# Performance work log

Hardware: AMD Instinct MI355X
Metric: run time of the kernel (lower is better)

The kernel has to match this reference:

```python
import jax, jax.numpy as jnp
import numpy as np

B, C, OUTC, H, W, K, P, S = 4, 64, 64, 128, 128, 3, 1, 1
KK = K * K


def setup_inputs() -> dict:
    key = jax.random.key(0)
    ks = jax.random.split(key, 5)
    x = jax.random.normal(ks[0], (B, C, H, W), dtype=jnp.float32)
    # small-scale offset weights keep learned offsets in a realistic few-pixel range
    w_off = jax.random.normal(ks[1], (2 * KK, C, 3, 3), dtype=jnp.float32) * 0.05
    b_off = jnp.zeros((2 * KK,), dtype=jnp.float32)
    w_mask = jax.random.normal(ks[2], (KK, C, 3, 3), dtype=jnp.float32) * 0.05
    b_mask = jnp.zeros((KK,), dtype=jnp.float32)
    w_dcn = jax.random.normal(ks[3], (OUTC, C, K, K), dtype=jnp.float32) * (1.0 / np.sqrt(C * KK))
    b_dcn = jnp.zeros((OUTC,), dtype=jnp.float32)
    return {"x": x, "w_off": w_off, "b_off": b_off, "w_mask": w_mask,
            "b_mask": b_mask, "w_dcn": w_dcn, "b_dcn": b_dcn}


def _conv3x3(x, w, b):
    y = jax.lax.conv_general_dilated(x, w, (1, 1), ((1, 1), (1, 1)),
                                     dimension_numbers=("NCHW", "OIHW", "NCHW"))
    return y + b[None, :, None, None]


def _deform_conv(x, offset, mask, w, b):
    # torchvision DeformConv2d (v2, modulated). offset layout: [B, kk, (dy,dx), H, W]
    Ho = (H + 2 * P - K) // S + 1
    Wo = (W + 2 * P - K) // S + 1
    off = offset.reshape(B, KK, 2, Ho, Wo)
    dy, dx = off[:, :, 0], off[:, :, 1]                      # [B,kk,Ho,Wo]
    ki, kj = jnp.meshgrid(jnp.arange(K), jnp.arange(K), indexing="ij")
    ki = ki.reshape(KK).astype(jnp.float32)
    kj = kj.reshape(KK).astype(jnp.float32)
    hg = (jnp.arange(Ho) * S - P).astype(jnp.float32)
    wg = (jnp.arange(Wo) * S - P).astype(jnp.float32)
    py = dy + ki[None, :, None, None] + hg[None, None, :, None]   # sample y coord
    px = dx + kj[None, :, None, None] + wg[None, None, None, :]   # sample x coord

    y0f = jnp.floor(py)
    x0f = jnp.floor(px)
    ly = py - y0f
    lx = px - x0f
    y0 = y0f.astype(jnp.int32)
    x0 = x0f.astype(jnp.int32)

    x_flat = x.reshape(B, C, H * W)

    def sample(yi, xi, wgt):
        valid = (yi >= 0) & (yi < H) & (xi >= 0) & (xi < W)
        idx = jnp.clip(yi, 0, H - 1) * W + jnp.clip(xi, 0, W - 1)  # [B,kk,Ho,Wo]
        g = jax.vmap(lambda xb, ib: xb[:, ib])(x_flat, idx)        # [B,C,kk,Ho,Wo]
        return g * (wgt * valid)[:, None]

    acc = (sample(y0, x0, (1 - ly) * (1 - lx))
           + sample(y0, x0 + 1, (1 - ly) * lx)
           + sample(y0 + 1, x0, ly * (1 - lx))
           + sample(y0 + 1, x0 + 1, ly * lx))                      # [B,C,kk,Ho,Wo]
    acc = acc * mask.reshape(B, 1, KK, Ho, Wo)
    out = jnp.einsum("bckhw,ock->bohw", acc, w.reshape(OUTC, C, KK))
    return out + b[None, :, None, None]


def reference(x, w_off, b_off, w_mask, b_mask, w_dcn, b_dcn):
    offset = _conv3x3(x, w_off, b_off)
    mask = jax.nn.sigmoid(_conv3x3(x, w_mask, b_mask))
    out = _deform_conv(x, offset, mask, w_dcn, b_dcn)
    return out, offset
```

## Files before the change

### kernel.cpp

```cpp
#include <hip/hip_runtime.h>
#include <hip/hip_bf16.h>
#include <math.h>

#define BB 4
#define CC 64
#define OCN 64
#define HH 128
#define WW 128
#define HW (HH*WW)
#define KKN 9
#define APAD 200

typedef short short8 __attribute__((ext_vector_type(8)));
typedef short short4v __attribute__((ext_vector_type(4)));
typedef float floatx4 __attribute__((ext_vector_type(4)));
typedef unsigned int uintx4 __attribute__((ext_vector_type(4)));

__device__ __forceinline__ float bf2f_us(unsigned short u) {
    return __uint_as_float(((unsigned)u) << 16);
}
__device__ __forceinline__ short f2bfs(float f) {
    __hip_bfloat16 h = __float2bfloat16(f);
    return *reinterpret_cast<short*>(&h);
}
__device__ __forceinline__ uintx4 as_u4(short8 v) {
    union { short8 s; uintx4 u; } x; x.s = v; return x.u;
}
__device__ __forceinline__ float blo(unsigned d) { return __uint_as_float(d << 16); }
__device__ __forceinline__ float bhi(unsigned d) { return __uint_as_float(d & 0xffff0000u); }

__global__ __launch_bounds__(256) void transpose_prep(
    const float* __restrict__ x,
    const float* __restrict__ w_dcn, const float* __restrict__ w_off,
    const float* __restrict__ b_off, const float* __restrict__ w_mask,
    const float* __restrict__ b_mask,
    __hip_bfloat16* __restrict__ xt, __hip_bfloat16* __restrict__ wTf,
    __hip_bfloat16* __restrict__ wOf, float* __restrict__ rebias)
{
    int blk = blockIdx.x;
    int tid = threadIdx.x;
    if (blk < BB * 512) {
        __shared__ float tile[64][33];
        int pixbase = (blk & 511) * 32;
        int b       = blk >> 9;
        const float* xb = x + (size_t)b * CC * HW;
        int p = tid & 31;
        #pragma unroll
        for (int i = 0; i < 8; ++i) {
            int c = (tid >> 5) * 8 + i;
            tile[c][p] = xb[(size_t)c * HW + pixbase + p];
        }
        __syncthreads();
        __hip_bfloat16* xo = xt + ((size_t)b * HW + pixbase) * CC;
        int pixl = tid >> 3;
        int c8t  = tid & 7;
        short8 o;
        #pragma unroll
        for (int i = 0; i < 8; ++i) o[i] = f2bfs(tile[c8t * 8 + i][pixl]);
        *reinterpret_cast<short8*>(&xo[(size_t)pixl * CC + c8t * 8]) = o;
        return;
    }
    int i = (blk - BB * 512) * 256 + tid;
    if (i < 18 * 4 * 64 * 8) {
        int jj = i & 7;
        int l  = (i >> 3) & 63;
        int nt = (i >> 9) & 3;
        int s  = i >> 11;
        int oc = nt * 16 + (l & 15);
        int kk = s * 32 + ((l >> 4) << 3) + jj;
        int c  = kk & 63;
        int kt = kk >> 6;
        wTf[i] = __float2bfloat16(w_dcn[(oc * CC + c) * 9 + kt]);
    }
    int j = i - 18 * 4 * 64 * 8;
    if (j >= 0 && j < 18 * 2 * 64 * 8) {
        int jj = j & 7;
        int l  = (j >> 3) & 63;
        int nt = (j >> 9) & 1;
        int s  = j >> 10;
        int oc = nt * 16 + (l & 15);
        int kk = s * 32 + ((l >> 4) << 3) + jj;
        int c  = kk & 63;
        int kt = kk >> 6;
        float v = 0.0f;
        if (oc < 18)      v = w_off[(oc * CC + c) * 9 + kt];
        else if (oc < 27) v = w_mask[((oc - 18) * CC + c) * 9 + kt];
        wOf[j] = __float2bfloat16(v);
    }
    int r = j - 18 * 2 * 64 * 8;
    if (r >= 0 && r < 27) rebias[r] = (r < 18) ? b_off[r] : b_mask[r - 18];
}

__global__ __launch_bounds__(256, 4) void deform_fused(
    const __hip_bfloat16* __restrict__ xt,
    const __hip_bfloat16* __restrict__ wTf, const __hip_bfloat16* __restrict__ wOf,
    const float* __restrict__ rebias, const float* __restrict__ b_dcn,
    float* __restrict__ off_out, float* __restrict__ out)
{
    __shared__ __align__(16) __hip_bfloat16 accs[64][APAD];
    __shared__ uintx4 tabs[KKN][64];
    __shared__ __hip_bfloat16 offs_l[18][68];
    __shared__ __hip_bfloat16 ms_l[KKN][68];

    int tid    = threadIdx.x;
    int lane   = tid & 63;
    int wv     = __builtin_amdgcn_readfirstlane(tid >> 6);
    int lane15 = lane & 15;
    int lq     = lane >> 4;
    int nt     = wv & 1;
    int ph     = wv >> 1;
    int pix    = tid >> 3;
    int c8     = tid & 7;
    int co     = c8 * 16;
    int kreg   = lq << 3;

    int wo0 = (blockIdx.x & 1) * 64;
    int row = (blockIdx.x >> 1) & (HH - 1);
    int b   = blockIdx.x >> 8;

    const char* xtb = (const char*)(xt + (size_t)b * HW * CC);
    const short8* wTf8 = (const short8*)wTf;
    const short8* wOf8 = (const short8*)wOf;
    const short8 zero8 = {0,0,0,0,0,0,0,0};

    floatx4 accomA[2] = {{0,0,0,0},{0,0,0,0}};
    for (int chunk = 0; chunk < 3; ++chunk) {
        int y = row + chunk - 1;
        bool yvalid = (unsigned)y < (unsigned)HH;
        int yc = min(max(y, 0), HH - 1);
        short8 v[2][3];
        #pragma unroll
        for (int h = 0; h < 2; ++h) {
            #pragma unroll
            for (int kl = 0; kl < 3; ++kl) {
                int xw = wo0 + h * 32 + pix + kl - 1;
                bool valid = yvalid && ((unsigned)xw < (unsigned)WW);
                int xc = min(max(xw, 0), WW - 1);
                short8 t = *(const short8*)(xtb + (((yc * WW) + xc) << 7) + co);
                v[h][kl] = valid ? t : zero8;
            }
        }
        #pragma unroll
        for (int h = 0; h < 2; ++h)
            #pragma unroll
            for (int kl = 0; kl < 3; ++kl)
                *reinterpret_cast<short8*>(&accs[h * 32 + pix][kl * 64 + c8 * 8]) = v[h][kl];
        __syncthreads();

        #pragma unroll
        for (int step = 0; step < 6; ++step) {
            int s = chunk * 6 + step;
            short8 bfrag = wOf8[(size_t)(s * 2 + nt) * 64 + lane];
            #pragma unroll
            for (int q = 0; q < 2; ++q) {
                int pg = ph * 2 + q;
                short8 a = *reinterpret_cast<const short8*>(&accs[pg * 16 + lane15][step * 32 + kreg]);
                accomA[q] = __builtin_amdgcn_mfma_f32_16x16x32_bf16(a, bfrag, accomA[q], 0, 0, 0);
            }
        }
        __syncthreads();
    }

    #pragma unroll
    for (int q = 0; q < 2; ++q) {
        int pg = ph * 2 + q;
        int pcl = pg * 16 + lq * 4;
        int oc = nt * 16 + lane15;
        if (oc < 18) {
            float bias = rebias[oc];
            floatx4 o = accomA[q];
            o[0] += bias; o[1] += bias; o[2] += bias; o[3] += bias;
            *reinterpret_cast<floatx4*>(
                &off_out[(((size_t)b * 18 + oc) * HH + row) * WW + wo0 + pcl]) = o;
            short4v ob = { f2bfs(o[0]), f2bfs(o[1]), f2bfs(o[2]), f2bfs(o[3]) };
            *reinterpret_cast<short4v*>(&offs_l[oc][pcl]) = ob;
        } else if (oc < 27) {
            float bias = rebias[oc];
            short4v mb;
            #pragma unroll
            for (int t = 0; t < 4; ++t)
                mb[t] = f2bfs(1.0f / (1.0f + expf(-(accomA[q][t] + bias))));
            *reinterpret_cast<short4v*>(&ms_l[oc - 18][pcl]) = mb;
        }
    }
    __syncthreads();

    for (int e = tid; e < KKN * 64; e += 256) {
        int k = e >> 6, p = e & 63;
        float dy = bf2f_us(*(const unsigned short*)&offs_l[2 * k][p]);
        float dx = bf2f_us(*(const unsigned short*)&offs_l[2 * k + 1][p]);
        float m  = bf2f_us(*(const unsigned short*)&ms_l[k][p]);
        float py = dy + (float)(k / 3) + (float)(row - 1);
        float px = dx + (float)(k % 3) + (float)(wo0 + p - 1);
        float y0f = floorf(py), x0f = floorf(px);
        float ly = py - y0f, lx = px - x0f;
        int y0 = (int)y0f, x0 = (int)x0f;
        uintx4 rec;
        #pragma unroll
        for (int t = 0; t < 4; ++t) {
            int yi = y0 + (t >> 1), xi = x0 + (t & 1);
            float wy = (t >> 1) ? ly : 1.0f - ly;
            float wx = (t & 1)  ? lx : 1.0f - lx;
            bool valid = ((unsigned)yi < (unsigned)HH) && ((unsigned)xi < (unsigned)WW);
            int yc2 = min(max(yi, 0), HH - 1);
            int xc2 = min(max(xi, 0), WW - 1);
            __hip_bfloat16 hw = __float2bfloat16(valid ? wy * wx * m : 0.0f);
            unsigned short wb = *reinterpret_cast<unsigned short*>(&hw);
            rec[t] = (unsigned)(yc2 * WW + xc2) | ((unsigned)wb << 16);
        }
        tabs[k][p] = rec;
    }
    __syncthreads();

    short8 buf[2][4];
    uintx4 tb[2];
    floatx4 accv[4] = {{0,0,0,0},{0,0,0,0},{0,0,0,0},{0,0,0,0}};

#define ISSUE(G) do { \
    uintx4 _t = tabs[(G) >> 1][pix + ((G) & 1) * 32]; \
    tb[(G) & 1] = _t; \
    buf[(G) & 1][0] = *(const short8*)(xtb + ((_t[0] & 0xffffu) << 7) + co); \
    buf[(G) & 1][1] = *(const short8*)(xtb + ((_t[1] & 0xffffu) << 7) + co); \
    buf[(G) & 1][2] = *(const short8*)(xtb + ((_t[2] & 0xffffu) << 7) + co); \
    buf[(G) & 1][3] = *(const short8*)(xtb + ((_t[3] & 0xffffu) << 7) + co); \
} while (0)

#define COMBINE(G) do { \
    float fA[8] = {0,0,0,0,0,0,0,0}; \
    _Pragma("unroll") \
    for (int t = 0; t < 4; ++t) { \
        float wt = __uint_as_float(tb[(G) & 1][t] & 0xffff0000u); \
        uintx4 dA = as_u4(buf[(G) & 1][t]); \
        _Pragma("unroll") \
        for (int jq = 0; jq < 4; ++jq) { \
            fA[2 * jq]     = fmaf(wt, blo(dA[jq]), fA[2 * jq]); \
            fA[2 * jq + 1] = fmaf(wt, bhi(dA[jq]), fA[2 * jq + 1]); \
        } \
    } \
    short8 oA; \
    _Pragma("unroll") \
    for (int jq = 0; jq < 8; ++jq) { oA[jq] = f2bfs(fA[jq]); } \
    *reinterpret_cast<short8*>( \
        &accs[((G) & 1) * 32 + pix][(((G) >> 1) % 3) * 64 + c8 * 8]) = oA; \
} while (0)

#define CMFMA(CH) do { \
    _Pragma("unroll") \
    for (int step = 0; step < 6; ++step) { \
        int s = (CH) * 6 + step; \
        short8 bfrag = wTf8[(size_t)(s * 4 + wv) * 64 + lane]; \
        _Pragma("unroll") \
        for (int pg = 0; pg < 4; ++pg) { \
            short8 a = *reinterpret_cast<const short8*>(&accs[pg * 16 + lane15][step * 32 + kreg]); \
            accv[pg] = __builtin_amdgcn_mfma_f32_16x16x32_bf16(a, bfrag, accv[pg], 0, 0, 0); \
        } \
    } \
} while (0)

    ISSUE(0); ISSUE(1);
    COMBINE(0); ISSUE(2);
    COMBINE(1); ISSUE(3);
    COMBINE(2); ISSUE(4);
    COMBINE(3); ISSUE(5);
    COMBINE(4); COMBINE(5);
    __syncthreads();
    ISSUE(6); ISSUE(7);
    CMFMA(0);
    asm volatile("s_waitcnt lgkmcnt(0)" ::: "memory");
    __builtin_amdgcn_s_barrier();
    COMBINE(6); ISSUE(8);
    COMBINE(7); ISSUE(9);
    COMBINE(8); ISSUE(10);
    COMBINE(9); ISSUE(11);
    COMBINE(10); COMBINE(11);
    __syncthreads();
    ISSUE(12); ISSUE(13);
    CMFMA(1);
    asm volatile("s_waitcnt lgkmcnt(0)" ::: "memory");
    __builtin_amdgcn_s_barrier();
    COMBINE(12); ISSUE(14);
    COMBINE(13); ISSUE(15);
    COMBINE(14); ISSUE(16);
    COMBINE(15); ISSUE(17);
    COMBINE(16); COMBINE(17);
    __syncthreads();
    CMFMA(2);

#undef ISSUE
#undef COMBINE
#undef CMFMA

    {
        int oc = wv * 16 + lane15;
        float bias = b_dcn[oc];
        #pragma unroll
        for (int pg = 0; pg < 4; ++pg) {
            int pcol = wo0 + pg * 16 + lq * 4;
            floatx4 o = accv[pg];
            o[0] += bias; o[1] += bias; o[2] += bias; o[3] += bias;
            *reinterpret_cast<floatx4*>(&out[(((size_t)b * OCN + oc) * HH + row) * WW + pcol]) = o;
        }
    }
}

extern "C" void kernel_launch(void* const* d_in, const int* in_sizes, int n_in,
                              void* d_out, int out_size, void* d_ws, size_t ws_size,
                              hipStream_t stream) {
    const float* x      = (const float*)d_in[0];
    const float* w_off  = (const float*)d_in[1];
    const float* b_off  = (const float*)d_in[2];
    const float* w_mask = (const float*)d_in[3];
    const float* b_mask = (const float*)d_in[4];
    const float* w_dcn  = (const float*)d_in[5];
    const float* b_dcn  = (const float*)d_in[6];

    float* out     = (float*)d_out;
    float* off_out = out + (size_t)BB * OCN * HW;

    float* rebias  = (float*)d_ws;
    __hip_bfloat16* xt  = (__hip_bfloat16*)(rebias + 32);
    __hip_bfloat16* wTf = xt + (size_t)BB * HW * CC;
    __hip_bfloat16* wOf = wTf + 18 * 4 * 64 * 8;

    int prep_total  = 18 * 4 * 64 * 8 + 18 * 2 * 64 * 8 + 27;
    int prep_blocks = (prep_total + 255) / 256;
    transpose_prep<<<BB * 512 + prep_blocks, 256, 0, stream>>>(
        x, w_dcn, w_off, b_off, w_mask, b_mask, xt, wTf, wOf, rebias);

    deform_fused<<<BB * HH * 2, 256, 0, stream>>>(
        xt, wTf, wOf, rebias, b_dcn, off_out, out);
}
```

Measured before the change: 39.96 us.

## Stage halo rows once for offset conv, double-buffer, and swizzle block order

The offset/mask 3x3 conv phase now stages one 66-pixel input row per kernel row into shared memory and reads the three horizontal taps as shifted views. The old code loaded three shifted copies of each row. Two LDS slots let the next row load while MFMAs run on the current one, which cuts the barriers from two per chunk to one. The block index is also swizzled so consecutive blocks map to rows spread across the image, which changes L2 locality. The new padded stride of 144 bytes may give different LDS bank behaviour.

```diff
diff --git a/kernel.cpp b/kernel.cpp
--- a/kernel.cpp
+++ b/kernel.cpp
@@ -10,6 +10,8 @@
 #define HW (HH*WW)
 #define KKN 9
 #define APAD 200
+#define RSTRIDE 144
+#define SLOTSZ (66*RSTRIDE)
 
 typedef short short8 __attribute__((ext_vector_type(8)));
 typedef short short4v __attribute__((ext_vector_type(4)));
@@ -97,7 +99,7 @@
     const float* __restrict__ rebias, const float* __restrict__ b_dcn,
     float* __restrict__ off_out, float* __restrict__ out)
 {
-    __shared__ __align__(16) __hip_bfloat16 accs[64][APAD];
+    __shared__ __align__(16) char scr[64 * APAD * 2];
     __shared__ uintx4 tabs[KKN][64];
     __shared__ __hip_bfloat16 offs_l[18][68];
     __shared__ __hip_bfloat16 ms_l[KKN][68];
@@ -114,9 +116,11 @@
     int co     = c8 * 16;
     int kreg   = lq << 3;
 
-    int wo0 = (blockIdx.x & 1) * 64;
-    int row = (blockIdx.x >> 1) & (HH - 1);
-    int b   = blockIdx.x >> 8;
+    int bid = blockIdx.x;
+    int swz = ((bid & 7) << 7) | (bid >> 3);
+    int wo0 = (swz & 1) * 64;
+    int row = (swz >> 1) & (HH - 1);
+    int b   = swz >> 8;
 
     const char* xtb = (const char*)(xt + (size_t)b * HW * CC);
     const short8* wTf8 = (const short8*)wTf;
@@ -124,42 +128,54 @@
     const short8 zero8 = {0,0,0,0,0,0,0,0};
 
     floatx4 accomA[2] = {{0,0,0,0},{0,0,0,0}};
-    for (int chunk = 0; chunk < 3; ++chunk) {
-        int y = row + chunk - 1;
-        bool yvalid = (unsigned)y < (unsigned)HH;
-        int yc = min(max(y, 0), HH - 1);
-        short8 v[2][3];
-        #pragma unroll
-        for (int h = 0; h < 2; ++h) {
-            #pragma unroll
-            for (int kl = 0; kl < 3; ++kl) {
-                int xw = wo0 + h * 32 + pix + kl - 1;
-                bool valid = yvalid && ((unsigned)xw < (unsigned)WW);
-                int xc = min(max(xw, 0), WW - 1);
-                short8 t = *(const short8*)(xtb + (((yc * WW) + xc) << 7) + co);
-                v[h][kl] = valid ? t : zero8;
-            }
-        }
-        #pragma unroll
-        for (int h = 0; h < 2; ++h)
-            #pragma unroll
-            for (int kl = 0; kl < 3; ++kl)
-                *reinterpret_cast<short8*>(&accs[h * 32 + pix][kl * 64 + c8 * 8]) = v[h][kl];
-        __syncthreads();
-
-        #pragma unroll
-        for (int step = 0; step < 6; ++step) {
-            int s = chunk * 6 + step;
-            short8 bfrag = wOf8[(size_t)(s * 2 + nt) * 64 + lane];
-            #pragma unroll
-            for (int q = 0; q < 2; ++q) {
-                int pg = ph * 2 + q;
-                short8 a = *reinterpret_cast<const short8*>(&accs[pg * 16 + lane15][step * 32 + kreg]);
-                accomA[q] = __builtin_amdgcn_mfma_f32_16x16x32_bf16(a, bfrag, accomA[q], 0, 0, 0);
-            }
-        }
-        __syncthreads();
-    }
+
+#define STAGE_ROW(KY, SLOT) do { \
+    int _y = row + (KY) - 1; \
+    bool _yv = (unsigned)_y < (unsigned)HH; \
+    int _yc = min(max(_y, 0), HH - 1); \
+    _Pragma("unroll") \
+    for (int _it = 0; _it < 3; ++_it) { \
+        int _e = tid + _it * 256; \
+        if (_e < 528) { \
+            int _px66 = _e >> 3, _c8 = _e & 7; \
+            int _xw = wo0 + _px66 - 1; \
+            bool _v = _yv && ((unsigned)_xw < (unsigned)WW); \
+            int _xc = min(max(_xw, 0), WW - 1); \
+            short8 _t = *(const short8*)(xtb + (((_yc * WW) + _xc) << 7) + _c8 * 16); \
+            if (!_v) _t = zero8; \
+            *(short8*)(scr + (SLOT) * SLOTSZ + _px66 * RSTRIDE + _c8 * 16) = _t; \
+        } \
+    } \
+} while (0)
+
+#define AMFMA(KY, SLOT) do { \
+    _Pragma("unroll") \
+    for (int s6 = 0; s6 < 6; ++s6) { \
+        int s = (KY) * 6 + s6; \
+        int kx = s6 >> 1; \
+        short8 bfrag = wOf8[(size_t)(s * 2 + nt) * 64 + lane]; \
+        _Pragma("unroll") \
+        for (int q = 0; q < 2; ++q) { \
+            int pg = ph * 2 + q; \
+            short8 a = *(const short8*)(scr + (SLOT) * SLOTSZ \
+                + (pg * 16 + lane15 + kx) * RSTRIDE + (s6 & 1) * 64 + lq * 16); \
+            accomA[q] = __builtin_amdgcn_mfma_f32_16x16x32_bf16(a, bfrag, accomA[q], 0, 0, 0); \
+        } \
+    } \
+} while (0)
+
+    STAGE_ROW(0, 0);
+    __syncthreads();
+    STAGE_ROW(1, 1);
+    AMFMA(0, 0);
+    __syncthreads();
+    STAGE_ROW(2, 0);
+    AMFMA(1, 1);
+    __syncthreads();
+    AMFMA(2, 0);
+
+#undef STAGE_ROW
+#undef AMFMA
 
     #pragma unroll
     for (int q = 0; q < 2; ++q) {
@@ -216,6 +232,8 @@
     uintx4 tb[2];
     floatx4 accv[4] = {{0,0,0,0},{0,0,0,0},{0,0,0,0},{0,0,0,0}};
 
+#define ACCS(PIX, COLB) (scr + (PIX) * (APAD * 2) + (COLB))
+
 #define ISSUE(G) do { \
     uintx4 _t = tabs[(G) >> 1][pix + ((G) & 1) * 32]; \
     tb[(G) & 1] = _t; \
@@ -240,8 +258,7 @@
     short8 oA; \
     _Pragma("unroll") \
     for (int jq = 0; jq < 8; ++jq) { oA[jq] = f2bfs(fA[jq]); } \
-    *reinterpret_cast<short8*>( \
-        &accs[((G) & 1) * 32 + pix][(((G) >> 1) % 3) * 64 + c8 * 8]) = oA; \
+    *(short8*)ACCS(((G) & 1) * 32 + pix, (((G) >> 1) % 3) * 128 + c8 * 16) = oA; \
 } while (0)
 
 #define CMFMA(CH) do { \
@@ -251,7 +268,7 @@
         short8 bfrag = wTf8[(size_t)(s * 4 + wv) * 64 + lane]; \
         _Pragma("unroll") \
         for (int pg = 0; pg < 4; ++pg) { \
-            short8 a = *reinterpret_cast<const short8*>(&accs[pg * 16 + lane15][step * 32 + kreg]); \
+            short8 a = *(const short8*)ACCS(pg * 16 + lane15, step * 64 + kreg * 2); \
             accv[pg] = __builtin_amdgcn_mfma_f32_16x16x32_bf16(a, bfrag, accv[pg], 0, 0, 0); \
         } \
     } \
@@ -289,6 +306,7 @@
 #undef ISSUE
 #undef COMBINE
 #undef CMFMA
+#undef ACCS
 
     {
         int oc = wv * 16 + lane15;
```

New measurement: 38.78 us. -3.0%, faster.
